# Performance work log

Measured on AMD Instinct MI355X. Metric: run time of the kernel, lower is better.

The kernel has to match this reference:

```python
import jax, jax.numpy as jnp
import numpy as np
from jax import lax

B, T, C, H, K = 8, 4096, 512, 512, 2


def setup_inputs() -> dict:
    key = jax.random.key(0)
    ks = jax.random.split(key, 4)
    scale = 1.0 / np.sqrt(K * C)
    return {
        "x": jax.random.normal(ks[0], (B, T, C), jnp.float32),
        "z_kernel": jax.random.normal(ks[1], (K, C, H), jnp.float32) * scale,
        "z_bias": jnp.zeros((H,), jnp.float32),
        "f_kernel": jax.random.normal(ks[2], (K, C, H), jnp.float32) * scale,
        "f_bias": jnp.zeros((H,), jnp.float32),
        "o_kernel": jax.random.normal(ks[3], (K, C, H), jnp.float32) * scale,
        "o_bias": jnp.zeros((H,), jnp.float32),
    }


def _conv1d(x, kernel, bias):
    # x: [B, T, C]; kernel: [K, C, H] (WIO); causal-left-padded input, VALID conv
    y = lax.conv_general_dilated(
        x, kernel, window_strides=(1,), padding="VALID",
        dimension_numbers=("NWC", "WIO", "NWC"))
    return y + bias


def reference(x, z_kernel, z_bias, f_kernel, f_bias, o_kernel, o_bias):
    k = z_kernel.shape[0]
    xp = jnp.pad(x, ((0, 0), (k - 1, 0), (0, 0)))  # causal pad on time axis
    z = jnp.tanh(_conv1d(xp, z_kernel, z_bias))            # [B, T, H]
    f = jax.nn.sigmoid(_conv1d(xp, f_kernel, f_bias))      # [B, T, H]
    o = jax.nn.sigmoid(_conv1d(xp, o_kernel, o_bias))      # [B, T, H]
    zin = (1.0 - f) * z  # fo-pooling: input gated by (1 - f)

    def step(h, zf):
        z_t, f_t = zf
        h_next = f_t * h + z_t
        return h_next, h_next

    init = jnp.zeros((x.shape[0], z.shape[-1]), z.dtype)
    _, hs = lax.scan(step, init, (jnp.swapaxes(zin, 0, 1), jnp.swapaxes(f, 0, 1)))
    hs = jnp.swapaxes(hs, 0, 1)  # [B, T, H]
    return hs * o
```

## Files before the change

### kernel.cpp

```cpp
#include <hip/hip_runtime.h>
#include <hip/hip_fp16.h>
#include <stdint.h>

#define Bb 8
#define Tt 4096
#define Cc 512
#define Hh 512
#define Mm (Bb*Tt)
#define Nn (3*Hh)
#define Kk (2*Cc)
#define NC 64
#define LC (Tt/NC)
#define XBS (Tt*Cc + Cc)
#define BK 64

typedef _Float16 half8 __attribute__((ext_vector_type(8)));
typedef _Float16 half4 __attribute__((ext_vector_type(4)));
typedef float  floatx4 __attribute__((ext_vector_type(4)));

typedef const __attribute__((address_space(1))) uint32_t* gptr_t;
typedef __attribute__((address_space(3))) uint32_t* lptr_t;

__device__ __forceinline__ void g2lds16(const void* g, void* l) {
    __builtin_amdgcn_global_load_lds((gptr_t)g, (lptr_t)l, 16, 0, 0);
}

__device__ __forceinline__ float fsigmoid(float x) {
    return 1.0f / (1.0f + __expf(-x));
}
__device__ __forceinline__ float ftanh(float x) {
    return 2.0f / (1.0f + __expf(-2.0f * x)) - 1.0f;
}

__global__ __launch_bounds__(256) void cvt_x(const float* __restrict__ x,
                                             _Float16* __restrict__ xh) {
    long i4 = ((long)blockIdx.x * 256 + threadIdx.x) * 4;
    int b = blockIdx.y;
    if (i4 >= XBS) return;
    half4 v;
    if (i4 >= Cc) {
        floatx4 xx = *(const floatx4*)&x[(long)b * (Tt*Cc) + i4 - Cc];
        v[0] = (_Float16)xx[0]; v[1] = (_Float16)xx[1];
        v[2] = (_Float16)xx[2]; v[3] = (_Float16)xx[3];
    } else {
        v[0] = v[1] = v[2] = v[3] = (_Float16)0.0f;
    }
    *(half4*)&xh[(long)b * XBS + i4] = v;
}

__global__ __launch_bounds__(256) void cvt_w(const float* __restrict__ zk,
                                             const float* __restrict__ fk,
                                             const float* __restrict__ ok,
                                             _Float16* __restrict__ bt) {
    int idx = blockIdx.x * 256 + threadIdx.x;
    int n  = idx >> 10;
    int kk = idx & 1023;
    int which = n >> 9;
    int h = n & 511;
    int kw = kk >> 9;
    int c = kk & 511;
    const float* src = (which == 0) ? zk : ((which == 1) ? fk : ok);
    bt[idx] = (_Float16)src[kw * (Cc*Hh) + c * Hh + h];
}

__global__ __launch_bounds__(256, 3) void gemm_qrnn(const _Float16* __restrict__ xh,
                                                    const _Float16* __restrict__ bt,
                                                    const float* __restrict__ zb,
                                                    const float* __restrict__ fb,
                                                    const float* __restrict__ ob,
                                                    _Float16* __restrict__ yh) {
    __shared__ _Float16 lA[128 * BK];
    __shared__ _Float16 lB[128 * BK];

    const int tid  = threadIdx.x;
    const int lane = tid & 63;
    const int w    = tid >> 6;
    const int m0   = blockIdx.x * 128;
    const int n0   = blockIdx.y * 128;
    const int wm   = (w & 1) * 64;
    const int wn   = (w >> 1) * 64;
    const int q    = lane >> 4;
    const int l15  = lane & 15;

    const int rl = lane >> 3;
    const int j  = lane & 7;
    const int jx = (j ^ rl) * 8;

    const _Float16* asrc[4];
    const _Float16* bsrc[4];
    _Float16* adst[4];
    _Float16* bdst[4];
#pragma unroll
    for (int i = 0; i < 4; ++i) {
        int r0 = w * 32 + i * 8;
        int rgA = m0 + r0 + rl;
        asrc[i] = xh + (((long)(rgA + (rgA >> 12))) << 9) + jx;
        int rgB = n0 + r0 + rl;
        bsrc[i] = bt + (((long)rgB) << 10) + jx;
        adst[i] = &lA[r0 * BK];
        bdst[i] = &lB[r0 * BK];
    }

    int aaddr[4], baddr[4];
    const int psw = (q ^ (l15 & 7)) * 8;
#pragma unroll
    for (int i = 0; i < 4; ++i) {
        aaddr[i] = (wm + i * 16 + l15) * BK + psw;
        baddr[i] = (wn + i * 16 + l15) * BK + psw;
    }

    floatx4 acc[4][4] = {};

    for (int kt = 0; kt < Kk / BK; ++kt) {
        const int kb = kt * BK;
#pragma unroll
        for (int i = 0; i < 4; ++i) g2lds16(asrc[i] + kb, adst[i]);
#pragma unroll
        for (int i = 0; i < 4; ++i) g2lds16(bsrc[i] + kb, bdst[i]);
        __syncthreads();

        half8 a0[4], a1[4], b0[4], b1[4];
#pragma unroll
        for (int i = 0; i < 4; ++i) {
            a0[i] = *(const half8*)&lA[aaddr[i]];
            a1[i] = *(const half8*)&lA[aaddr[i] ^ 32];
            b0[i] = *(const half8*)&lB[baddr[i]];
            b1[i] = *(const half8*)&lB[baddr[i] ^ 32];
        }
#pragma unroll
        for (int mi = 0; mi < 4; ++mi)
#pragma unroll
            for (int ni = 0; ni < 4; ++ni)
                acc[mi][ni] = __builtin_amdgcn_mfma_f32_16x16x32_f16(
                    a0[mi], b0[ni], acc[mi][ni], 0, 0, 0);
#pragma unroll
        for (int mi = 0; mi < 4; ++mi)
#pragma unroll
            for (int ni = 0; ni < 4; ++ni)
                acc[mi][ni] = __builtin_amdgcn_mfma_f32_16x16x32_f16(
                    a1[mi], b1[ni], acc[mi][ni], 0, 0, 0);
        __syncthreads();
    }

    const int gate = n0 >> 9;
    const float* bias = (gate == 0) ? zb : ((gate == 1) ? fb : ob);
    float bv[4];
#pragma unroll
    for (int ni = 0; ni < 4; ++ni)
        bv[ni] = bias[(n0 & 511) + wn + ni * 16 + l15];

#pragma unroll
    for (int mi = 0; mi < 4; ++mi) {
#pragma unroll
        for (int ni = 0; ni < 4; ++ni) {
#pragma unroll
            for (int r = 0; r < 4; ++r) {
                int m = m0 + wm + mi * 16 + q * 4 + r;
                int n = n0 + wn + ni * 16 + l15;
                float v = acc[mi][ni][r] + bv[ni];
                float a = (gate == 0) ? ftanh(v) : fsigmoid(v);
                yh[(long)m * Nn + n] = (_Float16)a;
            }
        }
    }
}

__global__ __launch_bounds__(64) void scan_partial(const _Float16* __restrict__ yh,
                                                   float* __restrict__ pf,
                                                   float* __restrict__ he) {
    int c = blockIdx.x & (NC - 1);
    int b = blockIdx.x >> 6;
    int lane = threadIdx.x;
    long base = ((long)(b * Tt + c * LC)) * Nn + lane * 8;
    float hl[8] = {0,0,0,0,0,0,0,0};
    float p[8]  = {1,1,1,1,1,1,1,1};
#pragma unroll 8
    for (int t = 0; t < LC; ++t) {
        half8 z8 = *(const half8*)&yh[base];
        half8 f8 = *(const half8*)&yh[base + 512];
#pragma unroll
        for (int jj = 0; jj < 8; ++jj) {
            float f = (float)f8[jj];
            hl[jj] = f * hl[jj] + (1.0f - f) * (float)z8[jj];
            p[jj] *= f;
        }
        base += Nn;
    }
    long o = ((long)(b * NC + c)) * Hh + lane * 8;
#pragma unroll
    for (int jj = 0; jj < 8; ++jj) { pf[o + jj] = p[jj]; he[o + jj] = hl[jj]; }
}

__global__ __launch_bounds__(256) void scan_combine(const float* __restrict__ pf,
                                                    const float* __restrict__ he,
                                                    float* __restrict__ hin) {
    int idx = blockIdx.x * 256 + threadIdx.x;
    int b = idx >> 9;
    int h = idx & 511;
    float hcur = 0.0f;
#pragma unroll 4
    for (int c = 0; c < NC; ++c) {
        int o = (b * NC + c) * Hh + h;
        hin[o] = hcur;
        hcur = pf[o] * hcur + he[o];
    }
}

__global__ __launch_bounds__(64) void scan_final(const _Float16* __restrict__ yh,
                                                 const float* __restrict__ hin,
                                                 float* __restrict__ out) {
    int c = blockIdx.x & (NC - 1);
    int b = blockIdx.x >> 6;
    int lane = threadIdx.x;
    long base  = ((long)(b * Tt + c * LC)) * Nn + lane * 8;
    long obase = ((long)(b * Tt + c * LC)) * Hh + lane * 8;
    long hb = ((long)(b * NC + c)) * Hh + lane * 8;
    float h[8];
#pragma unroll
    for (int jj = 0; jj < 8; ++jj) h[jj] = hin[hb + jj];
#pragma unroll 4
    for (int t = 0; t < LC; ++t) {
        half8 z8 = *(const half8*)&yh[base];
        half8 f8 = *(const half8*)&yh[base + 512];
        half8 o8 = *(const half8*)&yh[base + 1024];
#pragma unroll
        for (int jj = 0; jj < 8; ++jj) {
            float f = (float)f8[jj];
            h[jj] = f * h[jj] + (1.0f - f) * (float)z8[jj];
            out[obase + jj] = h[jj] * (float)o8[jj];
        }
        base += Nn;
        obase += Hh;
    }
}

extern "C" void kernel_launch(void* const* d_in, const int* in_sizes, int n_in,
                              void* d_out, int out_size, void* d_ws, size_t ws_size,
                              hipStream_t stream) {
    const float* x  = (const float*)d_in[0];
    const float* zk = (const float*)d_in[1];
    const float* zbias = (const float*)d_in[2];
    const float* fk = (const float*)d_in[3];
    const float* fbias = (const float*)d_in[4];
    const float* ok = (const float*)d_in[5];
    const float* obias = (const float*)d_in[6];
    float* out = (float*)d_out;

    char* ws = (char*)d_ws;
    _Float16* xh = (_Float16*)ws;
    _Float16* bt = (_Float16*)(ws + 33562624);
    _Float16* yh = (_Float16*)(ws + 36708352);
    float*    pf = (float*)(ws + 137371648);
    float*    he = (float*)(ws + 138420224);
    float*    hin= (float*)(ws + 139468800);

    cvt_x<<<dim3((XBS/4 + 255) / 256, Bb), 256, 0, stream>>>(x, xh);
    cvt_w<<<dim3((Nn * Kk) / 256), 256, 0, stream>>>(zk, fk, ok, bt);
    gemm_qrnn<<<dim3(Mm / 128, Nn / 128), 256, 0, stream>>>(xh, bt, zbias, fbias, obias, yh);
    scan_partial<<<dim3(Bb * NC), 64, 0, stream>>>(yh, pf, he);
    scan_combine<<<dim3(16), 256, 0, stream>>>(pf, he, hin);
    scan_final<<<dim3(Bb * NC), 64, 0, stream>>>(yh, hin, out);
}
```

Before: 312.8 us.

## Quadruple scan chunk count and transpose weight conversion through shared memory

Raises the number of time chunks per batch from 64 to 256, so the partial and final scan kernels launch four times as many blocks with shorter serial loops, giving more parallelism on the memory-bound scan. The weight convert kernel now transposes through a padded shared-memory tile so global reads and writes are coalesced, replacing the strided per-element gather. The scan scratch buffers are moved to the start of the workspace, reusing the fp16 input buffer that is dead after the GEMM. The trade-off is a longer sequential combine over 256 chunks in a 16-block kernel.

```diff
diff --git a/kernel.cpp b/kernel.cpp
--- a/kernel.cpp
+++ b/kernel.cpp
@@ -9,7 +9,7 @@
 #define Mm (Bb*Tt)
 #define Nn (3*Hh)
 #define Kk (2*Cc)
-#define NC 64
+#define NC 256
 #define LC (Tt/NC)
 #define XBS (Tt*Cc + Cc)
 #define BK 64
@@ -52,15 +52,31 @@
                                              const float* __restrict__ fk,
                                              const float* __restrict__ ok,
                                              _Float16* __restrict__ bt) {
-    int idx = blockIdx.x * 256 + threadIdx.x;
-    int n  = idx >> 10;
-    int kk = idx & 1023;
-    int which = n >> 9;
-    int h = n & 511;
-    int kw = kk >> 9;
-    int c = kk & 511;
+    __shared__ float tile[64][65];
+    const int c0 = (blockIdx.x & 7) * 64;
+    const int h0 = (blockIdx.x >> 3) * 64;
+    const int which = blockIdx.y >> 1;
+    const int kw    = blockIdx.y & 1;
     const float* src = (which == 0) ? zk : ((which == 1) ? fk : ok);
-    bt[idx] = (_Float16)src[kw * (Cc*Hh) + c * Hh + h];
+    src += kw * (Cc * Hh);
+    const int tr  = threadIdx.x >> 4;
+    const int tc4 = (threadIdx.x & 15) * 4;
+#pragma unroll
+    for (int i = 0; i < 4; ++i) {
+        int c = tr + i * 16;
+        floatx4 v = *(const floatx4*)&src[(long)(c0 + c) * Hh + h0 + tc4];
+        tile[c][tc4 + 0] = v[0]; tile[c][tc4 + 1] = v[1];
+        tile[c][tc4 + 2] = v[2]; tile[c][tc4 + 3] = v[3];
+    }
+    __syncthreads();
+#pragma unroll
+    for (int i = 0; i < 4; ++i) {
+        int h = tr + i * 16;
+        half4 o;
+#pragma unroll
+        for (int j = 0; j < 4; ++j) o[j] = (_Float16)tile[tc4 + j][h];
+        *(half4*)&bt[((long)(which * 512 + h0 + h) << 10) + kw * 512 + c0 + tc4] = o;
+    }
 }
 
 __global__ __launch_bounds__(256, 3) void gemm_qrnn(const _Float16* __restrict__ xh,
@@ -169,12 +185,12 @@
                                                    float* __restrict__ pf,
                                                    float* __restrict__ he) {
     int c = blockIdx.x & (NC - 1);
-    int b = blockIdx.x >> 6;
+    int b = blockIdx.x >> 8;
     int lane = threadIdx.x;
     long base = ((long)(b * Tt + c * LC)) * Nn + lane * 8;
     float hl[8] = {0,0,0,0,0,0,0,0};
     float p[8]  = {1,1,1,1,1,1,1,1};
-#pragma unroll 8
+#pragma unroll 4
     for (int t = 0; t < LC; ++t) {
         half8 z8 = *(const half8*)&yh[base];
         half8 f8 = *(const half8*)&yh[base + 512];
@@ -198,7 +214,7 @@
     int b = idx >> 9;
     int h = idx & 511;
     float hcur = 0.0f;
-#pragma unroll 4
+#pragma unroll 8
     for (int c = 0; c < NC; ++c) {
         int o = (b * NC + c) * Hh + h;
         hin[o] = hcur;
@@ -210,7 +226,7 @@
                                                  const float* __restrict__ hin,
                                                  float* __restrict__ out) {
     int c = blockIdx.x & (NC - 1);
-    int b = blockIdx.x >> 6;
+    int b = blockIdx.x >> 8;
     int lane = threadIdx.x;
     long base  = ((long)(b * Tt + c * LC)) * Nn + lane * 8;
     long obase = ((long)(b * Tt + c * LC)) * Hh + lane * 8;
@@ -250,12 +266,12 @@
     _Float16* xh = (_Float16*)ws;
     _Float16* bt = (_Float16*)(ws + 33562624);
     _Float16* yh = (_Float16*)(ws + 36708352);
-    float*    pf = (float*)(ws + 137371648);
-    float*    he = (float*)(ws + 138420224);
-    float*    hin= (float*)(ws + 139468800);
+    float*    pf = (float*)(ws);
+    float*    he = (float*)(ws + 4194304);
+    float*    hin= (float*)(ws + 8388608);
 
     cvt_x<<<dim3((XBS/4 + 255) / 256, Bb), 256, 0, stream>>>(x, xh);
-    cvt_w<<<dim3((Nn * Kk) / 256), 256, 0, stream>>>(zk, fk, ok, bt);
+    cvt_w<<<dim3(64, 6), 256, 0, stream>>>(zk, fk, ok, bt);
     gemm_qrnn<<<dim3(Mm / 128, Nn / 128), 256, 0, stream>>>(xh, bt, zbias, fbias, obias, yh);
     scan_partial<<<dim3(Bb * NC), 64, 0, stream>>>(yh, pf, he);
     scan_combine<<<dim3(16), 256, 0, stream>>>(pf, he, hin);
```

New measurement: 304.4 us. -2.7%, faster.
